# Kernel tuning notes

Hardware: AMD Instinct MI355X
Metric: run time of the kernel (lower is better)

Reference implementation:

```python
import jax, jax.numpy as jnp
import numpy as np

BS, A, C, H, W = 32, 3, 80, 64, 64
T = 50
IMG_W, IMG_H = 512.0, 512.0
ANCHORS = np.array([[10.0, 13.0], [16.0, 30.0], [33.0, 23.0]], dtype=np.float32)
IGNORE_THR = 0.5
LAMBDA_XY, LAMBDA_WH, LAMBDA_CONF, LAMBDA_CLS = 2.5, 2.5, 1.0, 1.0
EPS = 1e-12


def setup_inputs():
    key = jax.random.key(0)
    k1, k2, k3, k4 = jax.random.split(key, 4)
    inp = jax.random.normal(k1, (BS, A * (5 + C), H, W), dtype=jnp.float32)
    cls = jax.random.randint(k2, (BS, T, 1), 0, C).astype(jnp.float32)
    cxcy = jax.random.uniform(k3, (BS, T, 2), minval=0.05, maxval=0.95, dtype=jnp.float32)
    wh = jax.random.uniform(k4, (BS, T, 2), minval=0.02, maxval=0.3, dtype=jnp.float32)
    targets = jnp.concatenate([cls, cxcy, wh], axis=-1)  # [bs, T, 5] = (cls, cx, cy, w, h)
    return {"input": inp, "targets": targets}


def _iou_cxcywh(b1, b2):
    # b1, b2: [..., 4] in (cx, cy, w, h) format
    b1x1, b1x2 = b1[..., 0] - b1[..., 2] / 2, b1[..., 0] + b1[..., 2] / 2
    b1y1, b1y2 = b1[..., 1] - b1[..., 3] / 2, b1[..., 1] + b1[..., 3] / 2
    b2x1, b2x2 = b2[..., 0] - b2[..., 2] / 2, b2[..., 0] + b2[..., 2] / 2
    b2y1, b2y2 = b2[..., 1] - b2[..., 3] / 2, b2[..., 1] + b2[..., 3] / 2
    iw = jnp.clip(jnp.minimum(b1x2, b2x2) - jnp.maximum(b1x1, b2x1), 0.0)
    ih = jnp.clip(jnp.minimum(b1y2, b2y2) - jnp.maximum(b1y1, b2y1), 0.0)
    inter = iw * ih
    a1 = (b1x2 - b1x1) * (b1y2 - b1y1)
    a2 = (b2x2 - b2x1) * (b2y2 - b2y1)
    return inter / (a1 + a2 - inter + 1e-16)


def _bce(p, t):
    p = jnp.clip(p, EPS, 1.0 - EPS)
    return jnp.mean(-(t * jnp.log(p) + (1.0 - t) * jnp.log1p(-p)))


def _get_target(targets, scaled_anchors, pred_boxes):
    # Vectorized replacement of the per-object Python loop in get_target.
    bs, nt = targets.shape[0], targets.shape[1]
    valid = jnp.sum(targets, axis=-1) > 0  # [bs, T]
    gx = targets[..., 1] * W
    gy = targets[..., 2] * H
    gw = targets[..., 3] * W
    gh = targets[..., 4] * H
    gi = jnp.clip(gx.astype(jnp.int32), 0, W - 1)
    gj = jnp.clip(gy.astype(jnp.int32), 0, H - 1)
    # anchor IoU: both boxes centered at origin -> intersection = min(w)*min(h)
    aw, ah = scaled_anchors[:, 0], scaled_anchors[:, 1]  # [A]
    inter = jnp.minimum(gw[..., None], aw) * jnp.minimum(gh[..., None], ah)
    anch_iou = inter / (gw[..., None] * gh[..., None] + aw * ah - inter + 1e-16)  # [bs,T,A]
    best_n = jnp.argmax(anch_iou, axis=-1)  # [bs, T]
    # gather predicted boxes at each target's cell: [bs, T, A, 4]
    b_idx = jnp.broadcast_to(jnp.arange(bs)[:, None], (bs, nt))
    a_idx = jnp.arange(A)
    pb = pred_boxes[b_idx[:, :, None], a_idx[None, None, :], gj[:, :, None], gi[:, :, None]]
    gt_box = jnp.stack([gx, gy, gw, gh], axis=-1)[:, :, None, :]
    pred_iou = _iou_cxcywh(gt_box, pb)  # [bs, T, A]
    # scatter (invalid targets routed out of range and dropped)
    gi_s = jnp.where(valid, gi, W)
    shape = (bs, A, H, W)
    zeros = jnp.zeros(shape, dtype=jnp.float32)
    mask = zeros.at[b_idx, best_n, gj, gi_s].set(1.0, mode="drop")
    gi_no = jnp.where(valid[..., None] & (pred_iou > IGNORE_THR), gi[..., None], W)  # [bs,T,A]
    noobj = jnp.ones(shape, dtype=jnp.float32).at[
        b_idx[:, :, None], a_idx[None, None, :], gj[:, :, None], gi_no
    ].set(0.0, mode="drop")
    tx = zeros.at[b_idx, best_n, gj, gi_s].set(gx - gi, mode="drop")
    ty = zeros.at[b_idx, best_n, gj, gi_s].set(gy - gj, mode="drop")
    tw = zeros.at[b_idx, best_n, gj, gi_s].set(jnp.log(gw / aw[best_n] + 1e-16), mode="drop")
    th = zeros.at[b_idx, best_n, gj, gi_s].set(jnp.log(gh / ah[best_n] + 1e-16), mode="drop")
    gwxh = zeros.at[b_idx, best_n, gj, gi_s].set(
        jax.nn.sigmoid(gw) * jax.nn.sigmoid(gh), mode="drop")
    tconf = mask
    cls_i = jnp.clip(targets[..., 0].astype(jnp.int32), 0, C - 1)
    tcls = jnp.zeros(shape + (C,), dtype=jnp.float32).at[
        b_idx, best_n, gj, gi_s, cls_i].set(1.0, mode="drop")
    return mask, noobj, tx, ty, tw, th, gwxh, tconf, tcls


def _forward(input, targets):
    bs = input.shape[0]
    stride_w, stride_h = IMG_W / W, IMG_H / H
    scaled_anchors = jnp.asarray(ANCHORS) / jnp.array([stride_w, stride_h], dtype=jnp.float32)
    pred = input.reshape(bs, A, 5 + C, H, W).transpose(0, 1, 3, 4, 2)  # [bs,A,H,W,5+C]
    x = jax.nn.sigmoid(pred[..., 0])
    y = jax.nn.sigmoid(pred[..., 1])
    w = pred[..., 2]
    h = pred[..., 3]
    conf = jax.nn.sigmoid(pred[..., 4])
    pred_cls = jax.nn.sigmoid(pred[..., 5:])
    grid_x = jnp.arange(W, dtype=jnp.float32)[None, None, None, :]
    grid_y = jnp.arange(H, dtype=jnp.float32)[None, None, :, None]
    anchor_w = scaled_anchors[:, 0][None, :, None, None]
    anchor_h = scaled_anchors[:, 1][None, :, None, None]
    # .data in torch => detached decode
    pred_boxes = jax.lax.stop_gradient(jnp.stack([
        x + grid_x, y + grid_y, jnp.exp(w) * anchor_w, jnp.exp(h) * anchor_h
    ], axis=-1))  # [bs,A,H,W,4]
    tgt = _get_target(targets, scaled_anchors, pred_boxes)
    mask, noobj, tx, ty, tw, th, gwxh, tconf, tcls = [jax.lax.stop_gradient(t) for t in tgt]
    loss_x = _bce(x * mask, tx * mask)
    loss_y = _bce(y * mask, ty * mask)
    temp = (2.0 - gwxh) ** 2
    loss_w = jnp.mean((w * mask * temp - tw * mask * temp) ** 2)
    loss_h = jnp.mean((h * mask * temp - th * mask * temp) ** 2)
    loss_conf = _bce(conf * mask, mask) + 0.5 * _bce(conf * noobj, noobj * 0.0)
    # masked class BCE: equivalent to bce_loss(pred_cls[mask==1], tcls[mask==1])
    p = jnp.clip(pred_cls, EPS, 1.0 - EPS)
    e = -(tcls * jnp.log(p) + (1.0 - tcls) * jnp.log1p(-p))
    n_sel = jnp.sum(mask)
    loss_cls = jnp.sum(e * mask[..., None]) / (n_sel * C + 1e-16)
    loss = ((loss_x + loss_y) * LAMBDA_XY + (loss_w + loss_h) * LAMBDA_WH
            + loss_conf * LAMBDA_CONF + loss_cls * LAMBDA_CLS)
    return loss, loss_x, loss_y, loss_w, loss_h, loss_conf, loss_cls


def reference(input, targets):
    return _forward(input, targets)
```

## Files before the change

### kernel.cpp

```cpp
#include <hip/hip_runtime.h>
#include <math.h>

#define BSZ 32
#define NA 3
#define NC 80
#define HH 64
#define WW 64
#define NT 50
#define NCH (NA*(5+NC))

constexpr int NCELL = BSZ*NA*HH*WW;
constexpr float EPSf = 1e-12f;
constexpr float IGNORE_THR_C = 0.5f;
constexpr float CONST0 = 1e-12f;
constexpr float CLAMPB = 27.631021115928547f;

__device__ __forceinline__ float sigm(float x) { return 1.0f / (1.0f + __expf(-x)); }
__device__ __forceinline__ float softplus(float x) {
    return fmaxf(x, 0.0f) + __logf(1.0f + __expf(-fabsf(x)));
}
__device__ __forceinline__ float bce_t0(float v) { return fminf(softplus(v),  CLAMPB); }
__device__ __forceinline__ float bce_t1(float v) { return fminf(softplus(-v), CLAMPB); }

__global__ __launch_bounds__(64) void k_targets(const float* __restrict__ inp, const float* __restrict__ tgt,
                          unsigned char* __restrict__ mask_b, unsigned char* __restrict__ ignore_b,
                          float* __restrict__ txa, float* __restrict__ tya,
                          float* __restrict__ twa, float* __restrict__ tha,
                          float* __restrict__ gwa, unsigned int* __restrict__ clsbits)
{
    const int b = blockIdx.x;
    const int t = threadIdx.x;
    const float aw[3] = {1.25f, 2.0f, 4.125f};
    const float ah[3] = {1.625f, 3.75f, 2.875f};

    bool valid = false;
    int cell = -1, ci = 0, gi = 0, gj = 0, best = 0;
    float gx = 0, gy = 0, gw = 0, gh = 0;

    if (t < NT) {
        const float* tg = tgt + (size_t)(b*NT + t)*5;
        float c0 = tg[0], c1 = tg[1], c2 = tg[2], c3 = tg[3], c4 = tg[4];
        valid = (c0 + c1 + c2 + c3 + c4) > 0.0f;
        if (valid) {
            gx = c1 * WW; gy = c2 * HH; gw = c3 * WW; gh = c4 * HH;
            gi = min(max((int)gx, 0), WW-1);
            gj = min(max((int)gy, 0), HH-1);
            float bestiou = -1.0f;
            #pragma unroll
            for (int a = 0; a < 3; ++a) {
                float inter = fminf(gw, aw[a]) * fminf(gh, ah[a]);
                float iou = inter / (gw*gh + aw[a]*ah[a] - inter + 1e-16f);
                if (iou > bestiou) { bestiou = iou; best = a; }
            }
            cell = ((b*NA + best)*HH + gj)*WW + gi;
            ci = min(max((int)c0, 0), NC-1);
        }
    }

    if (valid) {
        #pragma unroll
        for (int a = 0; a < 3; ++a) {
            size_t base = (((size_t)b*NCH + a*(5+NC))*HH + gj)*WW + gi;
            const size_t PL = (size_t)HH*WW;
            float px = sigm(inp[base + 0*PL]) + (float)gi;
            float py = sigm(inp[base + 1*PL]) + (float)gj;
            float pw = __expf(inp[base + 2*PL]) * aw[a];
            float ph = __expf(inp[base + 3*PL]) * ah[a];

            float b1x1 = gx - gw*0.5f, b1x2 = gx + gw*0.5f;
            float b1y1 = gy - gh*0.5f, b1y2 = gy + gh*0.5f;
            float b2x1 = px - pw*0.5f, b2x2 = px + pw*0.5f;
            float b2y1 = py - ph*0.5f, b2y2 = py + ph*0.5f;
            float iw = fmaxf(fminf(b1x2,b2x2) - fmaxf(b1x1,b2x1), 0.0f);
            float ih = fmaxf(fminf(b1y2,b2y2) - fmaxf(b1y1,b2y1), 0.0f);
            float inter = iw*ih;
            float a1 = (b1x2-b1x1)*(b1y2-b1y1);
            float a2 = (b2x2-b2x1)*(b2y2-b2y1);
            float piou = inter / (a1 + a2 - inter + 1e-16f);
            if (piou > IGNORE_THR_C) {
                ignore_b[((b*NA + a)*HH + gj)*WW + gi] = 1;
            }
        }
    }

    bool winner = valid;
    unsigned int b0 = 0, b1 = 0, b2 = 0;
    for (int u = 0; u < NT; ++u) {
        int cu = __shfl(cell, u, 64);
        int vu = __shfl((int)valid, u, 64);
        int cu_ci = __shfl(ci, u, 64);
        if (vu && cu == cell) {
            if (u > t) winner = false;
            if (cu_ci < 32)      b0 |= 1u << cu_ci;
            else if (cu_ci < 64) b1 |= 1u << (cu_ci - 32);
            else                 b2 |= 1u << (cu_ci - 64);
        }
    }

    if (winner) {
        mask_b[cell] = 1;
        clsbits[cell*3+0] = b0;
        clsbits[cell*3+1] = b1;
        clsbits[cell*3+2] = b2;
        txa[cell] = gx - (float)gi;
        tya[cell] = gy - (float)gj;
        twa[cell] = logf(gw / aw[best] + 1e-16f);
        tha[cell] = logf(gh / ah[best] + 1e-16f);
        gwa[cell] = sigm(gw) * sigm(gh);
    }
}

__global__ __launch_bounds__(256) void k_loss(const float* __restrict__ inp,
                       const unsigned char* __restrict__ mask_b,
                       const unsigned char* __restrict__ ignore_b,
                       const float* __restrict__ txa, const float* __restrict__ tya,
                       const float* __restrict__ twa, const float* __restrict__ tha,
                       const float* __restrict__ gwa,
                       const unsigned int* __restrict__ clsbits,
                       double* __restrict__ sums)
{
    const int tid = blockIdx.x * blockDim.x + threadIdx.x;
    const int n0 = tid * 4;
    float s[8] = {0,0,0,0,0,0,0,0};

    {
        int i0 = n0 & (WW-1);
        int j  = (n0 >> 6) & (HH-1);
        int a  = (n0 >> 12) % NA;
        int b  = n0 / (NA*HH*WW);
        size_t base = (((size_t)b*NCH + a*(5+NC))*HH + j)*WW + i0;
        const size_t PL = (size_t)HH*WW;

        float4 conf4 = *reinterpret_cast<const float4*>(inp + base + 4*PL);
        unsigned int m4  = *reinterpret_cast<const unsigned int*>(mask_b + n0);
        unsigned int ig4 = *reinterpret_cast<const unsigned int*>(ignore_b + n0);
        const float cv[4] = {conf4.x, conf4.y, conf4.z, conf4.w};

        #pragma unroll
        for (int e = 0; e < 4; ++e) {
            float v = cv[e];
            bool m  = ((m4  >> (8*e)) & 0xff) != 0;
            bool ig = ((ig4 >> (8*e)) & 0xff) != 0;

            s[5] += ig ? CONST0 : bce_t0(v);

            if (m) {
                int n = n0 + e;
                size_t be = base + e;
                float xv = inp[be + 0*PL];
                float yv = inp[be + 1*PL];
                float w  = inp[be + 2*PL];
                float h  = inp[be + 3*PL];
                float tx = txa[n], ty = tya[n], tw = twa[n], th = tha[n];
                float gwxh = gwa[n];

                s[0] += tx*bce_t1(xv) + (1.0f - tx)*bce_t0(xv);
                s[1] += ty*bce_t1(yv) + (1.0f - ty)*bce_t0(yv);

                float temp = (2.0f - gwxh); temp = temp*temp;
                float dw = (w - tw) * temp;  s[2] += dw*dw;
                float dh = (h - th) * temp;  s[3] += dh*dh;

                s[4] += bce_t1(v);

                unsigned int bb0 = clsbits[n*3+0], bb1 = clsbits[n*3+1], bb2 = clsbits[n*3+2];
                float sc = 0.0f;
                for (int c = 0; c < NC; ++c) {
                    float p = inp[be + (size_t)(5+c)*PL];
                    unsigned int word = (c < 32) ? bb0 : ((c < 64) ? bb1 : bb2);
                    bool tc = (word >> (c & 31)) & 1u;
                    sc += tc ? bce_t1(p) : bce_t0(p);
                }
                s[6] += sc;
                s[7] += 1.0f;
            } else {
                s[0] += CONST0; s[1] += CONST0; s[4] += CONST0;
            }
        }
    }

    #pragma unroll
    for (int k = 0; k < 8; ++k) {
        float v = s[k];
        for (int off = 32; off > 0; off >>= 1) v += __shfl_down(v, off, 64);
        s[k] = v;
    }
    __shared__ float sh[4][8];
    int lane = threadIdx.x & 63, wv = threadIdx.x >> 6;
    if (lane == 0) {
        #pragma unroll
        for (int k = 0; k < 8; ++k) sh[wv][k] = s[k];
    }
    __syncthreads();
    if (threadIdx.x == 0) {
        #pragma unroll
        for (int k = 0; k < 8; ++k) {
            double v = (double)sh[0][k] + (double)sh[1][k] + (double)sh[2][k] + (double)sh[3][k];
            atomicAdd(&sums[k], v);
        }
    }
}

__global__ void k_final(const double* __restrict__ sums, float* __restrict__ out)
{
    if (blockIdx.x != 0 || threadIdx.x != 0) return;
    double N = (double)NCELL;
    double lx = sums[0] / N;
    double ly = sums[1] / N;
    double lw = sums[2] / N;
    double lh = sums[3] / N;
    double lconf = sums[4] / N + 0.5 * (sums[5] / N);
    double lcls  = sums[6] / (sums[7] * NC + 1e-16);
    double loss = (lx + ly) * 2.5 + (lw + lh) * 2.5 + lconf * 1.0 + lcls * 1.0;
    out[0] = (float)loss;
    out[1] = (float)lx;
    out[2] = (float)ly;
    out[3] = (float)lw;
    out[4] = (float)lh;
    out[5] = (float)lconf;
    out[6] = (float)lcls;
}

extern "C" void kernel_launch(void* const* d_in, const int* in_sizes, int n_in,
                              void* d_out, int out_size, void* d_ws, size_t ws_size,
                              hipStream_t stream)
{
    const float* inp = (const float*)d_in[0];
    const float* tgt = (const float*)d_in[1];
    float* out = (float*)d_out;

    char* ws = (char*)d_ws;
    double* sums           = (double*)ws;
    unsigned char* mask_b  = (unsigned char*)(ws + 64);
    unsigned char* ignore_b= mask_b + NCELL;
    float* txa  = (float*)(ws + 64 + 2*(size_t)NCELL);
    float* tya  = txa + NCELL;
    float* twa  = tya + NCELL;
    float* tha  = twa + NCELL;
    float* gwa  = tha + NCELL;
    unsigned int* clsbits = (unsigned int*)(gwa + NCELL);

    hipMemsetAsync(ws, 0, 64 + 2*(size_t)NCELL, stream);

    k_targets<<<BSZ, 64, 0, stream>>>(inp, tgt, mask_b, ignore_b, txa, tya, twa, tha, gwa, clsbits);

    int nthreads = NCELL / 4;
    k_loss<<<nthreads/256, 256, 0, stream>>>(inp, mask_b, ignore_b, txa, tya, twa, tha, gwa, clsbits, sums);

    k_final<<<1, 64, 0, stream>>>(sums, out);
}
```

Before: 244.4 us.

## Distribute per-cell class BCE across wavefront lanes and add constant padding at finalization

The loss kernel now assigns one cell per thread instead of four with float4 loads. For each masked cell in a wavefront, the 80-class BCE is spread across the 64 lanes using ballot and shuffle, then reduced with xor-shuffles, replacing the serial 80-iteration loop run by a single lane. The constant epsilon padding for unmasked cells is moved to the final kernel as an analytic term. This targets divergence and serialized strided loads for the sparse masked cells, at the cost of four times as many threads and losing the vectorized conf, mask and ignore loads.

```diff
diff --git a/kernel.cpp b/kernel.cpp
--- a/kernel.cpp
+++ b/kernel.cpp
@@ -10,7 +10,6 @@
 #define NCH (NA*(5+NC))
 
 constexpr int NCELL = BSZ*NA*HH*WW;
-constexpr float EPSf = 1e-12f;
 constexpr float IGNORE_THR_C = 0.5f;
 constexpr float CONST0 = 1e-12f;
 constexpr float CLAMPB = 27.631021115928547f;
@@ -119,66 +118,76 @@
                        const unsigned int* __restrict__ clsbits,
                        double* __restrict__ sums)
 {
-    const int tid = blockIdx.x * blockDim.x + threadIdx.x;
-    const int n0 = tid * 4;
-    float s[8] = {0,0,0,0,0,0,0,0};
-
-    {
-        int i0 = n0 & (WW-1);
-        int j  = (n0 >> 6) & (HH-1);
-        int a  = (n0 >> 12) % NA;
-        int b  = n0 / (NA*HH*WW);
-        size_t base = (((size_t)b*NCH + a*(5+NC))*HH + j)*WW + i0;
-        const size_t PL = (size_t)HH*WW;
-
-        float4 conf4 = *reinterpret_cast<const float4*>(inp + base + 4*PL);
-        unsigned int m4  = *reinterpret_cast<const unsigned int*>(mask_b + n0);
-        unsigned int ig4 = *reinterpret_cast<const unsigned int*>(ignore_b + n0);
-        const float cv[4] = {conf4.x, conf4.y, conf4.z, conf4.w};
-
-        #pragma unroll
-        for (int e = 0; e < 4; ++e) {
-            float v = cv[e];
-            bool m  = ((m4  >> (8*e)) & 0xff) != 0;
-            bool ig = ((ig4 >> (8*e)) & 0xff) != 0;
-
-            s[5] += ig ? CONST0 : bce_t0(v);
-
-            if (m) {
-                int n = n0 + e;
-                size_t be = base + e;
-                float xv = inp[be + 0*PL];
-                float yv = inp[be + 1*PL];
-                float w  = inp[be + 2*PL];
-                float h  = inp[be + 3*PL];
-                float tx = txa[n], ty = tya[n], tw = twa[n], th = tha[n];
-                float gwxh = gwa[n];
-
-                s[0] += tx*bce_t1(xv) + (1.0f - tx)*bce_t0(xv);
-                s[1] += ty*bce_t1(yv) + (1.0f - ty)*bce_t0(yv);
-
-                float temp = (2.0f - gwxh); temp = temp*temp;
-                float dw = (w - tw) * temp;  s[2] += dw*dw;
-                float dh = (h - th) * temp;  s[3] += dh*dh;
-
-                s[4] += bce_t1(v);
-
-                unsigned int bb0 = clsbits[n*3+0], bb1 = clsbits[n*3+1], bb2 = clsbits[n*3+2];
-                float sc = 0.0f;
-                for (int c = 0; c < NC; ++c) {
-                    float p = inp[be + (size_t)(5+c)*PL];
-                    unsigned int word = (c < 32) ? bb0 : ((c < 64) ? bb1 : bb2);
-                    bool tc = (word >> (c & 31)) & 1u;
-                    sc += tc ? bce_t1(p) : bce_t0(p);
-                }
-                s[6] += sc;
-                s[7] += 1.0f;
-            } else {
-                s[0] += CONST0; s[1] += CONST0; s[4] += CONST0;
-            }
-        }
-    }
-
+    const int n = blockIdx.x * blockDim.x + threadIdx.x;
+    const int lane = threadIdx.x & 63;
+    const size_t PL = (size_t)HH*WW;
+
+    int i = n & (WW-1);
+    int j = (n >> 6) & (HH-1);
+    int a = (n >> 12) % NA;
+    int b = n / (NA*HH*WW);
+    size_t base = (((size_t)b*NCH + a*(5+NC))*HH + j)*WW + i;
+
+    float conf = inp[base + 4*PL];
+    bool m  = mask_b[n]   != 0;
+    bool ig = ignore_b[n] != 0;
+
+    float s0=0, s1=0, s2=0, s3=0, s4=0, s6=0, s7=0;
+    float s5 = ig ? CONST0 : bce_t0(conf);
+
+    unsigned int bb0 = 0, bb1 = 0, bb2 = 0;
+    if (m) {
+        float xv = inp[base + 0*PL];
+        float yv = inp[base + 1*PL];
+        float w  = inp[base + 2*PL];
+        float h  = inp[base + 3*PL];
+        float tx = txa[n], ty = tya[n], tw = twa[n], th = tha[n];
+        float gwxh = gwa[n];
+
+        s0 = tx*bce_t1(xv) + (1.0f - tx)*bce_t0(xv);
+        s1 = ty*bce_t1(yv) + (1.0f - ty)*bce_t0(yv);
+        float temp = (2.0f - gwxh); temp = temp*temp;
+        float dw = (w - tw) * temp;  s2 = dw*dw;
+        float dh = (h - th) * temp;  s3 = dh*dh;
+        s4 = bce_t1(conf);
+        s7 = 1.0f;
+        bb0 = clsbits[n*3+0]; bb1 = clsbits[n*3+1]; bb2 = clsbits[n*3+2];
+    }
+
+    unsigned long long mb = __ballot(m);
+    while (mb) {
+        int src = __ffsll((long long)mb) - 1;
+        mb &= mb - 1;
+        int ns  = __shfl(n, src, 64);
+        unsigned int c0 = __shfl(bb0, src, 64);
+        unsigned int c1 = __shfl(bb1, src, 64);
+        unsigned int c2 = __shfl(bb2, src, 64);
+
+        int is = ns & (WW-1);
+        int js = (ns >> 6) & (HH-1);
+        int as_ = (ns >> 12) % NA;
+        int bs = ns / (NA*HH*WW);
+        size_t sbase = (((size_t)bs*NCH + as_*(5+NC))*HH + js)*WW + is;
+
+        float part;
+        {
+            int c = lane;
+            float p = inp[sbase + (size_t)(5+c)*PL];
+            bool tc = (((c < 32) ? c0 : c1) >> (c & 31)) & 1u;
+            part = tc ? bce_t1(p) : bce_t0(p);
+        }
+        if (lane < NC - 64) {
+            int c = 64 + lane;
+            float p = inp[sbase + (size_t)(5+c)*PL];
+            bool tc = (c2 >> lane) & 1u;
+            part += tc ? bce_t1(p) : bce_t0(p);
+        }
+        #pragma unroll
+        for (int off = 32; off > 0; off >>= 1) part += __shfl_xor(part, off, 64);
+        if (lane == src) s6 += part;
+    }
+
+    float s[8] = {s0, s1, s2, s3, s4, s5, s6, s7};
     #pragma unroll
     for (int k = 0; k < 8; ++k) {
         float v = s[k];
@@ -186,7 +195,7 @@
         s[k] = v;
     }
     __shared__ float sh[4][8];
-    int lane = threadIdx.x & 63, wv = threadIdx.x >> 6;
+    int wv = threadIdx.x >> 6;
     if (lane == 0) {
         #pragma unroll
         for (int k = 0; k < 8; ++k) sh[wv][k] = s[k];
@@ -205,12 +214,14 @@
 {
     if (blockIdx.x != 0 || threadIdx.x != 0) return;
     double N = (double)NCELL;
-    double lx = sums[0] / N;
-    double ly = sums[1] / N;
+    double nsel = sums[7];
+    double cpad = (double)CONST0 * (N - nsel);
+    double lx = (sums[0] + cpad) / N;
+    double ly = (sums[1] + cpad) / N;
     double lw = sums[2] / N;
     double lh = sums[3] / N;
-    double lconf = sums[4] / N + 0.5 * (sums[5] / N);
-    double lcls  = sums[6] / (sums[7] * NC + 1e-16);
+    double lconf = (sums[4] + cpad) / N + 0.5 * (sums[5] / N);
+    double lcls  = sums[6] / (nsel * NC + 1e-16);
     double loss = (lx + ly) * 2.5 + (lw + lh) * 2.5 + lconf * 1.0 + lcls * 1.0;
     out[0] = (float)loss;
     out[1] = (float)lx;
@@ -244,8 +255,7 @@
 
     k_targets<<<BSZ, 64, 0, stream>>>(inp, tgt, mask_b, ignore_b, txa, tya, twa, tha, gwa, clsbits);
 
-    int nthreads = NCELL / 4;
-    k_loss<<<nthreads/256, 256, 0, stream>>>(inp, mask_b, ignore_b, txa, tya, twa, tha, gwa, clsbits, sums);
+    k_loss<<<NCELL/256, 256, 0, stream>>>(inp, mask_b, ignore_b, txa, tya, twa, tha, gwa, clsbits, sums);
 
     k_final<<<1, 64, 0, stream>>>(sums, out);
 }
```

Measured after the change: 326.0 us. +33.4%, slower.
